# Kernel optimization log

Hardware: AMD Instinct MI355X
Metric: run time of the kernel (lower is better)

The kernel has to match this reference:

```python
import jax, jax.numpy as jnp
import numpy as np
from jax.scipy.linalg import cholesky, solve_triangular, cho_solve

N, M, D = 16384, 2048, 8
VAR, LS = 1.0, 0.5      # RBF kernel hyperparameters (same for kernel_f and kernel_g)
JITTER = 1e-6
BATCH_RATE = 1.0
HALF_LOG_2PI = 0.5 * float(np.log(2.0 * np.pi))


def rbf(x1, x2):
    # K[i,j] = VAR * exp(-||x1_i - x2_j||^2 / (2 LS^2))
    d2 = (jnp.sum(x1 * x1, 1)[:, None] + jnp.sum(x2 * x2, 1)[None, :]
          - 2.0 * (x1 @ x2.T))
    return VAR * jnp.exp(-0.5 * d2 / (LS * LS))


def setup_inputs() -> dict:
    key = jax.random.key(0)
    ks = jax.random.split(key, 7)
    x = jax.random.normal(ks[0], (N, D), dtype=jnp.float32)
    y = jax.random.normal(ks[1], (N, 1), dtype=jnp.float32)
    z = 2.0 * jax.random.uniform(ks[2], (M, D), dtype=jnp.float32) - 1.0  # inducing inputs in [-1,1]^D
    q_m_f = 0.5 * jax.random.normal(ks[3], (M, 1), dtype=jnp.float32)
    q_m_g = 0.5 * jax.random.normal(ks[4], (M, 1), dtype=jnp.float32)
    # Cholesky-like params: identity plus small strictly-lower noise -> PD covariance
    q_L_f = jnp.eye(M, dtype=jnp.float32) + 0.01 * jnp.tril(
        jax.random.normal(ks[5], (M, M), dtype=jnp.float32), -1)
    q_L_g = jnp.eye(M, dtype=jnp.float32) + 0.01 * jnp.tril(
        jax.random.normal(ks[6], (M, M), dtype=jnp.float32), -1)
    return {"x": x, "y": y, "z": z, "q_m_f": q_m_f, "q_L_f": q_L_f,
            "q_m_g": q_m_g, "q_L_g": q_L_g}


def _gp_marginals_and_kl(x, z, q_m, q_L_raw):
    """Marginal posterior mean/var at x and KL(q(u)||p(u)) for one sparse GP."""
    L_S = jnp.tril(q_L_raw)                     # [M,M]
    Kuu = rbf(z, z) + JITTER * jnp.eye(M, dtype=x.dtype)
    Lk = cholesky(Kuu, lower=True)
    Kfu = rbf(x, z)                             # [N,M]
    # A = Kfu @ Kuu^{-1}
    A = cho_solve((Lk, True), Kfu.T).T          # [N,M]
    m = (A @ q_m)[:, 0]                         # [N]
    # diag(Kff + A (S - Kuu) A^T) = diag(Kff) + diag(A S A^T) - diag(Kfu A^T)
    S = L_S @ L_S.T
    diag_Kff = jnp.full((x.shape[0],), VAR, dtype=x.dtype)
    v = diag_Kff + jnp.sum((A @ S) * A, axis=1) - jnp.sum(A * Kfu, axis=1)
    # KL(N(q_m, S) || N(0, Kuu))
    alpha = solve_triangular(Lk, q_m, lower=True)       # Kuu^{-1/2} m
    W = solve_triangular(Lk, L_S, lower=True)           # Kuu^{-1/2} L_S
    logdet_K = 2.0 * jnp.sum(jnp.log(jnp.diag(Lk)))
    logdet_S = 2.0 * jnp.sum(jnp.log(jnp.abs(jnp.diag(L_S))))
    kl = 0.5 * (jnp.sum(W * W) + jnp.sum(alpha * alpha)
                - jnp.asarray(M, x.dtype) + logdet_K - logdet_S)
    return m, v, kl


def reference(x, y, z, q_m_f, q_L_f, q_m_g, q_L_g):
    m_f, v_f, kl_f = _gp_marginals_and_kl(x, z, q_m_f, q_L_f)
    m_g, v_g, kl_g = _gp_marginals_and_kl(x, z, q_m_g, q_L_g)
    yv = y[:, 0]
    # HetGaussian variational expectation (Saul et al. 2016):
    # E_q[log N(y | f, exp(g))] per point
    expectation = (-HALF_LOG_2PI - 0.5 * m_g
                   - 0.5 * ((yv - m_f) ** 2 + v_f) * jnp.exp(-m_g + 0.5 * v_g))
    elbo = BATCH_RATE * jnp.sum(expectation) - (kl_f + kl_g)
    return -elbo
```

## Files before the change

### kernel.cpp

```cpp
#include <hip/hip_runtime.h>
#include <math.h>

#define NN 16384
#define MM 2048
#define DD 8
#define NB 32
#define GRIDN 256
#define SZB ((size_t)16777216)

constexpr float HLOG2PI = 0.91893853320467274178f;

using short8  = __attribute__((ext_vector_type(8))) short;
using float4v = __attribute__((ext_vector_type(4))) float;

__device__ __forceinline__ float4v f4zero(){ float4v v; v[0]=0.f; v[1]=0.f; v[2]=0.f; v[3]=0.f; return v; }

__device__ __forceinline__ void bfsplit(float v, short& h, short& lo){
  unsigned b = __float_as_uint(v);
  h = (short)(b >> 16);
  float hf = __uint_as_float(b & 0xFFFF0000u);
  lo = (short)(__float_as_uint(v - hf) >> 16);
}
__device__ __forceinline__ float bf2f(short s){
  return __uint_as_float(((unsigned)(unsigned short)s) << 16);
}
__device__ __forceinline__ float4v mfma3(short8 ah, short8 al, short8 bh, short8 bl, float4v c){
  c = __builtin_amdgcn_mfma_f32_16x16x32_bf16(ah, bh, c, 0, 0, 0);
  c = __builtin_amdgcn_mfma_f32_16x16x32_bf16(ah, bl, c, 0, 0, 0);
  c = __builtin_amdgcn_mfma_f32_16x16x32_bf16(al, bh, c, 0, 0, 0);
  return c;
}

__device__ __forceinline__ void gbar0(int* cnt, int* flag, int& gen){
  __syncthreads();
  if (threadIdx.x == 0){
    ++gen;
    __builtin_amdgcn_fence(__ATOMIC_RELEASE, "agent");
    int old = __hip_atomic_fetch_add(cnt, 1, __ATOMIC_RELAXED, __HIP_MEMORY_SCOPE_AGENT);
    if (old == gen*GRIDN - 1){
      __builtin_amdgcn_fence(__ATOMIC_ACQ_REL, "agent");
      __hip_atomic_store(flag, gen, __ATOMIC_RELAXED, __HIP_MEMORY_SCOPE_AGENT);
    } else {
      while (__hip_atomic_load(flag, __ATOMIC_RELAXED, __HIP_MEMORY_SCOPE_AGENT) < gen)
        __builtin_amdgcn_s_sleep(8);
    }
    __builtin_amdgcn_fence(__ATOMIC_ACQUIRE, "agent");
  }
  __syncthreads();
}

__device__ __forceinline__ void gbar_h(int* bar, int xcc, int myN, int nxcd, int& gen){
  __syncthreads();
  if (threadIdx.x == 0){
    ++gen;
    int* lcnt  = bar + xcc*32;
    int* lflag = bar + 512 + xcc*32;
    int* gcnt  = bar + 1024;
    int* gflag = bar + 1056;
    int old = __hip_atomic_fetch_add(lcnt, 1, __ATOMIC_RELAXED, __HIP_MEMORY_SCOPE_AGENT);
    if (old == gen*myN - 1){
      __builtin_amdgcn_fence(__ATOMIC_RELEASE, "agent");
      int g = __hip_atomic_fetch_add(gcnt, 1, __ATOMIC_RELAXED, __HIP_MEMORY_SCOPE_AGENT);
      if (g == gen*nxcd - 1){
        __hip_atomic_store(gflag, gen, __ATOMIC_RELAXED, __HIP_MEMORY_SCOPE_AGENT);
      } else {
        while (__hip_atomic_load(gflag, __ATOMIC_RELAXED, __HIP_MEMORY_SCOPE_AGENT) < gen)
          __builtin_amdgcn_s_sleep(8);
      }
      __builtin_amdgcn_fence(__ATOMIC_ACQUIRE, "agent");
      __hip_atomic_store(lflag, gen, __ATOMIC_RELAXED, __HIP_MEMORY_SCOPE_AGENT);
    } else {
      while (__hip_atomic_load(lflag, __ATOMIC_RELAXED, __HIP_MEMORY_SCOPE_AGENT) < gen)
        __builtin_amdgcn_s_sleep(8);
      __builtin_amdgcn_fence(__ATOMIC_ACQUIRE, "agent");
    }
  }
  __syncthreads();
}

__device__ __forceinline__ float block_reduce(float v, float* scratch){
  int lane = threadIdx.x & 63;
  int w    = threadIdx.x >> 6;
  #pragma unroll
  for (int off=32; off; off>>=1) v += __shfl_down(v, off, 64);
  __syncthreads();
  if (lane==0) scratch[w] = v;
  __syncthreads();
  float r = 0.f;
  if (threadIdx.x < 4) r = scratch[threadIdx.x];
  if (w==0){ r += __shfl_down(r, 2, 64); r += __shfl_down(r, 1, 64); }
  return r;
}

__device__ __forceinline__ void stage64(float (*S)[68], const float* __restrict__ g, int ld, int t){
  #pragma unroll
  for (int p=t; p<1024; p+=256)
    *(float4*)&S[p>>4][(p&15)*4] = *(const float4*)&g[(size_t)(p>>4)*ld + (p&15)*4];
}
__device__ __forceinline__ void tile_gemm_step(float acc[4][4], const float (*As)[68], const float (*Bs)[68], int tx, int ty){
  for (int k=0;k<64;++k){
    float ar[4], bc4[4];
    #pragma unroll
    for (int u=0;u<4;++u){ ar[u]=As[ty*4+u][k]; bc4[u]=Bs[k][tx*4+u]; }
    #pragma unroll
    for (int u=0;u<4;++u)
      #pragma unroll
      for (int v=0;v<4;++v) acc[u][v] += ar[u]*bc4[v];
  }
}
__device__ __forceinline__ void tile_syrk_step(float acc[4][4], const float (*P)[68], const float (*Q)[68], int tx, int ty){
  for (int k=0;k<64;++k){
    float pr[4], qc[4];
    #pragma unroll
    for (int u=0;u<4;++u){ pr[u]=P[ty*4+u][k]; qc[u]=Q[tx*4+u][k]; }
    #pragma unroll
    for (int u=0;u<4;++u)
      #pragma unroll
      for (int v=0;v<4;++v) acc[u][v] += pr[u]*qc[v];
  }
}

__device__ __forceinline__ void factor64_reg(const float (*S)[68],
    float* __restrict__ lkd, float* __restrict__ sdg_, int d, int t){
  if (t < 64){
    float xr[64];
    #pragma unroll
    for (int c4=0;c4<16;++c4) *(float4*)&xr[c4*4] = *(const float4*)&S[t][c4*4];
    float myrp = 1.f;
    #pragma unroll
    for (int j=0;j<64;++j){
      float ajj = __shfl(xr[j], j, 64);
      float piv = sqrtf(fmaxf(ajj, 1e-20f));
      float rp  = 1.f/piv;
      float val = xr[j]*rp;
      if (t==j){ xr[j] = piv; myrp = rp; }
      else if (t>j) xr[j] = val;
      else val = 0.f;
      #pragma unroll
      for (int c=j+1;c<64;++c){
        float vc = __shfl(val, c, 64);
        if (c<=t) xr[c] -= val*vc;
      }
    }
    #pragma unroll
    for (int c=0;c<64;++c) if (c>t) xr[c] = 0.f;
    #pragma unroll
    for (int c4=0;c4<16;++c4)
      *(float4*)&lkd[d*4096 + t*64 + c4*4] = *(float4*)&xr[c4*4];
    sdg_[d*64 + t] = myrp;
  }
}

__global__ __launch_bounds__(256) void factor_coop(
    const float* __restrict__ z,
    const float* __restrict__ qlf, const float* __restrict__ qlg,
    const float* __restrict__ qmf, const float* __restrict__ qmg,
    float* __restrict__ kuu, float* __restrict__ linv,
    float* __restrict__ wf, float* __restrict__ wg,
    float* __restrict__ af, float* __restrict__ ag,
    float* __restrict__ ptmp, float* __restrict__ lkdiag,
    float* __restrict__ sdg, float* __restrict__ ltri, int* __restrict__ bar)
{
  __shared__ float As[64][68];
  __shared__ float Bs[64][68];
  __shared__ float Cs[64][68];
  __shared__ float sd[64];
  __shared__ int binfo[2];
  const int bid = blockIdx.x, t = threadIdx.x;
  const int tx = t & 15, ty = t >> 4;

  int xcc_r;
  asm volatile("s_getreg_b32 %0, hwreg(HW_REG_XCC_ID)" : "=s"(xcc_r));
  const int xcc = xcc_r & 15;
  if (t == 0)
    __hip_atomic_fetch_add(bar + 1152 + xcc*32, 1, __ATOMIC_RELAXED, __HIP_MEMORY_SCOPE_AGENT);
  int gen0 = 0;
  gbar0(bar + 1088, bar + 1120, gen0);
  if (t == 0){
    int myN = __hip_atomic_load(bar + 1152 + xcc*32, __ATOMIC_RELAXED, __HIP_MEMORY_SCOPE_AGENT);
    int nx = 0;
    for (int i=0;i<16;++i)
      nx += (__hip_atomic_load(bar + 1152 + i*32, __ATOMIC_RELAXED, __HIP_MEMORY_SCOPE_AGENT) > 0);
    binfo[0] = myN; binfo[1] = nx;
  }
  __syncthreads();
  const int myN = binfo[0], nxcd = binfo[1];
  int gen = 0;

  if (bid == 0){
    for (int p=t; p<128; p+=256){ int i=p>>1, h=p&1;
      *(float4*)&As[i][h*4] = *(const float4*)&z[(size_t)i*DD + h*4]; }
    __syncthreads();
    float kv[4][4];
    #pragma unroll
    for (int u=0;u<4;++u)
      #pragma unroll
      for (int v=0;v<4;++v){
        float d2=0.f;
        #pragma unroll
        for (int d=0;d<8;++d){ float df=As[ty*4+u][d]-As[tx*4+v][d]; d2+=df*df; }
        kv[u][v] = __expf(-2.f*d2) + ((ty*4+u)==(tx*4+v) ? 1e-6f : 0.f);
      }
    __syncthreads();
    #pragma unroll
    for (int u=0;u<4;++u)
      #pragma unroll
      for (int v=0;v<4;++v) As[ty*4+u][tx*4+v] = kv[u][v];
    __syncthreads();
    factor64_reg(As, lkdiag, sdg, 0, t);
  } else {
    for (int idx=bid; idx<528; idx+=GRIDN-1){
      int r=0; while ((r+1)*(r+2)/2 <= idx) ++r;
      int c = idx - r*(r+1)/2;
      __syncthreads();
      for (int p=t; p<128; p+=256){ int i=p>>1, h=p&1;
        *(float4*)&As[i][h*4] = *(const float4*)&z[(size_t)(r*64+i)*DD + h*4];
        *(float4*)&Bs[i][h*4] = *(const float4*)&z[(size_t)(c*64+i)*DD + h*4]; }
      __syncthreads();
      #pragma unroll
      for (int u=0;u<4;++u){
        float4 o;
        float* ov = (float*)&o;
        #pragma unroll
        for (int v=0;v<4;++v){
          float d2=0.f;
          #pragma unroll
          for (int d=0;d<8;++d){ float df=As[ty*4+u][d]-Bs[tx*4+v][d]; d2+=df*df; }
          float val = __expf(-2.f*d2);
          if (r*64+ty*4+u == c*64+tx*4+v) val += 1e-6f;
          ov[v] = val;
        }
        *(float4*)&kuu[(size_t)(r*64+ty*4+u)*MM + c*64 + tx*4] = o;
      }
    }
  }
  gbar_h(bar, xcc, myN, nxcd, gen);

  for (int kb=0; kb<31; ++kb){
    int T = NB-1 - kb;
    int ntiles = T*(T+1)/2;
    if (bid < ntiles){
      stage64(Cs, lkdiag + kb*4096, 64, t);
      if (t < 64) sd[t] = sdg[kb*64 + t];
    }
    for (int idx=bid; idx<ntiles; idx+=GRIDN){
      int r=0; while ((r+1)*(r+2)/2 <= idx) ++r;
      int c = idx - r*(r+1)/2;
      int bi = kb+1+r, bc = kb+1+c;
      __syncthreads();
      stage64(As, kuu + (size_t)(bi*64)*MM + kb*64, MM, t);
      if (bc != bi) stage64(Bs, kuu + (size_t)(bc*64)*MM + kb*64, MM, t);
      __syncthreads();
      {
        int w = t>>6, l = t&63;
        if (w==0 || (w==1 && bc!=bi)){
          float (*S)[68] = (w==0)? As : Bs;
          float xr[64];
          #pragma unroll
          for (int c4=0;c4<16;++c4) *(float4*)&xr[c4*4] = *(const float4*)&S[l][c4*4];
          #pragma unroll
          for (int j=0;j<64;++j){
            float xj = xr[j]*sd[j];
            xr[j] = xj;
            #pragma unroll
            for (int cc=j+1;cc<64;++cc) xr[cc] -= xj*Cs[cc][j];
          }
          #pragma unroll
          for (int c4=0;c4<16;++c4) *(float4*)&S[l][c4*4] = *(float4*)&xr[c4*4];
        }
      }
      __syncthreads();
      if (bc == kb+1){
        for (int p=t;p<1024;p+=256)
          *(float4*)&ltri[(size_t)(bi*64+(p>>4))*MM + kb*64 + (p&15)*4] =
              *(float4*)&As[p>>4][(p&15)*4];
      }
      float acc[4][4] = {};
      tile_syrk_step(acc, As, (bc==bi)? As : Bs, tx, ty);
      if (bi==kb+1 && bc==kb+1){
        __syncthreads();
        #pragma unroll
        for (int u=0;u<4;++u)
          #pragma unroll
          for (int v=0;v<4;++v) Bs[ty*4+u][tx*4+v] = acc[u][v];
        __syncthreads();
        for (int p=t;p<1024;p+=256){
          int i=p>>4, c4=p&15;
          float4 kv = *(const float4*)&kuu[(size_t)(bi*64+i)*MM + bi*64 + c4*4];
          float4 bv = *(float4*)&Bs[i][c4*4];
          float4 o; o.x=kv.x-bv.x; o.y=kv.y-bv.y; o.z=kv.z-bv.z; o.w=kv.w-bv.w;
          *(float4*)&As[i][c4*4] = o;
        }
        __syncthreads();
        factor64_reg(As, lkdiag, sdg, kb+1, t);
      } else {
        #pragma unroll
        for (int u=0;u<4;++u){
          float4* dst = (float4*)&kuu[(size_t)(bi*64+ty*4+u)*MM + bc*64 + tx*4];
          float4 o = *dst;
          o.x-=acc[u][0]; o.y-=acc[u][1]; o.z-=acc[u][2]; o.w-=acc[u][3];
          *dst = o;
        }
      }
    }
    gbar_h(bar, xcc, myN, nxcd, gen);
  }

  if (bid < NB){
    stage64(As, lkdiag + bid*4096, 64, t);
    __syncthreads();
    if (t < 64){
      for (int j=0;j<64;++j){
        float s = (j==t)?1.f:0.f;
        for (int k=t;k<j;++k) s -= As[j][k]*Bs[k][t];
        Bs[j][t] = (j>=t)? s/As[j][j] : 0.f;
      }
    }
    __syncthreads();
    for (int p=t;p<1024;p+=256){ int i=p>>4, c4=p&15;
      *(float4*)&linv[(size_t)(bid*64+i)*MM + bid*64 + c4*4] = *(float4*)&Bs[i][c4*4]; }
  }
  gbar_h(bar, xcc, myN, nxcd, gen);

  for (int idx=bid; idx<16; idx+=GRIDN){
    int m = idx;
    __syncthreads();
    stage64(As, ltri + (size_t)((2*m+1)*64)*MM + (2*m)*64, MM, t);
    stage64(Bs, linv + (size_t)((2*m)*64)*MM   + (2*m)*64, MM, t);
    __syncthreads();
    float acc[4][4]={};
    tile_gemm_step(acc, As, Bs, tx, ty);
    __syncthreads();
    #pragma unroll
    for (int u=0;u<4;++u)
      #pragma unroll
      for (int v=0;v<4;++v) Bs[ty*4+u][tx*4+v] = acc[u][v];
    stage64(As, linv + (size_t)((2*m+1)*64)*MM + (2*m+1)*64, MM, t);
    __syncthreads();
    float o[4][4]={};
    tile_gemm_step(o, As, Bs, tx, ty);
    #pragma unroll
    for (int u=0;u<4;++u)
      *(float4*)&linv[(size_t)((2*m+1)*64+ty*4+u)*MM + (2*m)*64 + tx*4] =
          make_float4(-o[u][0],-o[u][1],-o[u][2],-o[u][3]);
  }
  gbar_h(bar, xcc, myN, nxcd, gen);

  for (int m=bid; m<8; m+=GRIDN){
    float* pm = ptmp + (size_t)m*128*128;
    for (int ti=0; ti<2; ++ti)
      for (int tj=0; tj<2; ++tj){
        int rb = m*4 + 2 + ti, cb0 = m*4;
        float acc[4][4]={};
        for (int k=tj; k<2; ++k){
          __syncthreads();
          stage64(As, ltri + (size_t)(rb*64)*MM + (cb0+k)*64, MM, t);
          stage64(Bs, linv + (size_t)((cb0+k)*64)*MM + (cb0+tj)*64, MM, t);
          __syncthreads();
          tile_gemm_step(acc, As, Bs, tx, ty);
        }
        #pragma unroll
        for (int u=0;u<4;++u)
          *(float4*)&pm[(size_t)(ti*64+ty*4+u)*128 + tj*64 + tx*4] =
              make_float4(acc[u][0],acc[u][1],acc[u][2],acc[u][3]);
      }
    for (int ti=0; ti<2; ++ti)
      for (int tj=0; tj<2; ++tj){
        int rb = m*4 + 2 + ti;
        float acc[4][4]={};
        for (int k=0; k<=ti; ++k){
          __syncthreads();
          stage64(As, linv + (size_t)(rb*64)*MM + (m*4+2+k)*64, MM, t);
          stage64(Bs, pm + (size_t)(k*64)*128 + tj*64, 128, t);
          __syncthreads();
          tile_gemm_step(acc, As, Bs, tx, ty);
        }
        #pragma unroll
        for (int u=0;u<4;++u)
          *(float4*)&linv[(size_t)(rb*64+ty*4+u)*MM + (m*4+tj)*64 + tx*4] =
              make_float4(-acc[u][0],-acc[u][1],-acc[u][2],-acc[u][3]);
      }
  }
  gbar_h(bar, xcc, myN, nxcd, gen);

  for (int s=2; s<5; ++s){
    int nb = 1<<s, mc = 16>>s, b = 64<<s;
    int tiles = mc*nb*nb;
    for (int idx=bid; idx<tiles; idx+=GRIDN){
      int m = idx/(nb*nb), r2 = idx%(nb*nb);
      int ti = r2/nb, tj = r2%nb;
      int rb = m*2*nb + nb + ti, cb0 = m*2*nb;
      float acc[4][4]={};
      for (int k=tj; k<nb; ++k){
        __syncthreads();
        stage64(As, ltri + (size_t)(rb*64)*MM + (cb0+k)*64, MM, t);
        stage64(Bs, linv + (size_t)((cb0+k)*64)*MM + (cb0+tj)*64, MM, t);
        __syncthreads();
        tile_gemm_step(acc, As, Bs, tx, ty);
      }
      float* pm = ptmp + (size_t)m*b*b;
      #pragma unroll
      for (int u=0;u<4;++u)
        *(float4*)&pm[(size_t)(ti*64+ty*4+u)*b + tj*64 + tx*4] =
            make_float4(acc[u][0],acc[u][1],acc[u][2],acc[u][3]);
    }
    gbar_h(bar, xcc, myN, nxcd, gen);
    for (int idx=bid; idx<tiles; idx+=GRIDN){
      int m = idx/(nb*nb), r2 = idx%(nb*nb);
      int ti = r2/nb, tj = r2%nb;
      int rb = m*2*nb + nb + ti;
      const float* pm = ptmp + (size_t)m*b*b;
      float acc[4][4]={};
      for (int k=0; k<=ti; ++k){
        __syncthreads();
        stage64(As, linv + (size_t)(rb*64)*MM + (m*2*nb+nb+k)*64, MM, t);
        stage64(Bs, pm + (size_t)(k*64)*b + tj*64, b, t);
        __syncthreads();
        tile_gemm_step(acc, As, Bs, tx, ty);
      }
      #pragma unroll
      for (int u=0;u<4;++u)
        *(float4*)&linv[(size_t)(rb*64+ty*4+u)*MM + (m*2*nb+tj)*64 + tx*4] =
            make_float4(-acc[u][0],-acc[u][1],-acc[u][2],-acc[u][3]);
    }
    gbar_h(bar, xcc, myN, nxcd, gen);
  }

  for (int idx=bid; idx<2*528; idx+=GRIDN){
    int gp = idx/528, rem = idx%528;
    int bi=0; while ((bi+1)*(bi+2)/2 <= rem) ++bi;
    int bj = rem - bi*(bi+1)/2;
    const float* ql = gp ? qlg : qlf;
    float* w        = gp ? wg  : wf;
    float acc[4][4]={};
    for (int bk=bj; bk<=bi; ++bk){
      __syncthreads();
      stage64(As, linv + (size_t)(bi*64)*MM + bk*64, MM, t);
      stage64(Bs, ql   + (size_t)(bk*64)*MM + bj*64, MM, t);
      __syncthreads();
      if (bk==bj){
        for (int p=t;p<4096;p+=256){ int i=p>>6, c=p&63; if (i<c) Bs[i][c]=0.f; }
        __syncthreads();
      }
      tile_gemm_step(acc, As, Bs, tx, ty);
    }
    #pragma unroll
    for (int u=0;u<4;++u)
      *(float4*)&w[(size_t)(bi*64+ty*4+u)*MM + bj*64 + tx*4] =
          make_float4(acc[u][0],acc[u][1],acc[u][2],acc[u][3]);
  }
  {
    int gw = bid*4 + (t>>6), l = t&63;
    for (int job=gw; job<4096; job+=GRIDN*4){
      int gp = job>>11, r = job&2047;
      const float* qm = gp ? qmg : qmf;
      float s=0.f;
      for (int c=l; c<=r; c+=64) s += linv[(size_t)r*MM+c]*qm[c];
      #pragma unroll
      for (int off=32; off; off>>=1) s += __shfl_down(s, off, 64);
      if (l==0) (gp ? ag : af)[r] = s;
    }
  }
}


__global__ __launch_bounds__(256) void zfrag_kernel(const float* __restrict__ z,
    short* __restrict__ zfh, short* __restrict__ zfl, float* __restrict__ zn2){
  int zr = blockIdx.x*256 + threadIdx.x;
  float v[DD]; float s = 0.f;
  #pragma unroll
  for (int d=0; d<DD; ++d){ v[d] = z[zr*DD + d]; s += v[d]*v[d]; }
  zn2[zr] = s;
  size_t base = (size_t)(zr >> 4)*512 + (zr & 15)*32;
  #pragma unroll
  for (int k=0; k<32; ++k){
    short h = 0, lo = 0;
    if (k < DD) bfsplit(v[k], h, lo);
    zfh[base + k] = h; zfl[base + k] = lo;
  }
}

__global__ __launch_bounds__(256) void red_small(const float* __restrict__ lkd,
    const float* __restrict__ qlf, const float* __restrict__ qlg,
    const float* __restrict__ af, const float* __restrict__ ag,
    float* __restrict__ scal){
  __shared__ float scratch[4];
  float ldk=0, ldf=0, ldg=0, a2f=0, a2g=0;
  for (int i=threadIdx.x;i<MM;i+=256){
    int kb = i>>6, r = i&63;
    ldk += __logf(lkd[kb*4096 + r*64 + r]);
    ldf += __logf(fabsf(qlf[(size_t)i*MM+i]));
    ldg += __logf(fabsf(qlg[(size_t)i*MM+i]));
    float v = af[i]; a2f += v*v;
    v = ag[i];       a2g += v*v;
  }
  float r;
  r = block_reduce(ldk, scratch); if (threadIdx.x==0) scal[0] = 2.f*r;
  r = block_reduce(ldf, scratch); if (threadIdx.x==0) scal[1] = 2.f*r;
  r = block_reduce(ldg, scratch); if (threadIdx.x==0) scal[2] = 2.f*r;
  r = block_reduce(a2f, scratch); if (threadIdx.x==0) scal[3] = r;
  r = block_reduce(a2g, scratch); if (threadIdx.x==0) scal[4] = r;
}

__global__ __launch_bounds__(256) void redw_kernel(const float* __restrict__ wf,
    const float* __restrict__ wg, float* __restrict__ scal){
  __shared__ float scratch[4];
  size_t start  = (size_t)blockIdx.x*256 + threadIdx.x;
  size_t stride = (size_t)gridDim.x*256;
  float sf=0, sg=0;
  for (size_t p=start;p<(size_t)MM*MM;p+=stride){
    float v=wf[p]; sf += v*v;
    v=wg[p];       sg += v*v;
  }
  float r = block_reduce(sf, scratch);
  if (threadIdx.x==0) atomicAdd(&scal[5], r);
  r = block_reduce(sg, scratch);
  if (threadIdx.x==0) atomicAdd(&scal[6], r);
}

__global__ void kl_kernel(const float* __restrict__ scal, float* __restrict__ out){
  float klf = 0.5f*(scal[5] + scal[3] - (float)MM + scal[0] - scal[1]);
  float klg = 0.5f*(scal[6] + scal[4] - (float)MM + scal[0] - scal[2]);
  out[0] += klf + klg;
}

__global__ __launch_bounds__(256) void split_rowmajor(const float* __restrict__ src,
    short* __restrict__ dh, short* __restrict__ dl){
  int p = blockIdx.x*256 + threadIdx.x;
  int chunk = p >> 9, wi = p & 511;
  int mo = chunk >> 6, ko = chunk & 63;
  int row = mo*16 + (wi >> 5), col = ko*32 + (wi & 31);
  float v = src[(size_t)row*MM + col];
  short h, lo; bfsplit(v, h, lo);
  dh[p] = h; dl[p] = lo;
}

__global__ __launch_bounds__(256) void split_transpose(const float* __restrict__ src,
    short* __restrict__ dh, short* __restrict__ dl){
  __shared__ float tile[32][33];
  int t = threadIdx.x;
  int mb = blockIdx.x, kb = blockIdx.y;
  #pragma unroll
  for (int k=0;k<4;++k){
    int idx = t + k*256;
    int lr = idx >> 5, lc = idx & 31;
    tile[lr][lc] = src[(size_t)(kb*32+lr)*MM + mb*32 + lc];
  }
  __syncthreads();
  #pragma unroll
  for (int e=0;e<4;++e){
    int p = t*4 + e;
    int c = p >> 9, wi = p & 511;
    int i = (wi >> 5) & 15, kk = wi & 31;
    float v = tile[kk][c*16 + i];
    short h, lo; bfsplit(v, h, lo);
    size_t gp = ((size_t)(mb*2 + c)*64 + kb)*512 + wi;
    dh[gp] = h; dl[gp] = lo;
  }
}

__global__ __launch_bounds__(256, 2) void tt_mfma(
    const float* __restrict__ x, const float* __restrict__ zn2,
    const short* __restrict__ zfh, const short* __restrict__ zfl,
    const short* __restrict__ lvh, const short* __restrict__ lvl,
    short* __restrict__ tth, short* __restrict__ ttl){
  __shared__ __align__(16) short lAh[8192], lAl[8192], lBh[8192], lBl[8192];
  int t = threadIdx.x;
  int l = t & 63, w = t >> 6;
  int istrip = blockIdx.x, bj2 = blockIdx.y;
  int li = l & 15, q = l >> 4;
  int lofs = li*32 + q*8;
  int wn4 = (w>>1)*4, wm4 = (w&1)*4;

  short8 xh[2], xl[2];
  float xn2v[8];
  {
    float xn2t[2];
    #pragma unroll
    for (int tn=0; tn<2; ++tn){
      int n = istrip*128 + w*32 + tn*16 + li;
      const float4* xp = (const float4*)(x + (size_t)n*DD);
      float4 p0 = xp[0], p1 = xp[1];
      float v[8] = {p0.x,p0.y,p0.z,p0.w,p1.x,p1.y,p1.z,p1.w};
      float s = 0.f;
      #pragma unroll
      for (int d=0; d<8; ++d) s += v[d]*v[d];
      xn2t[tn] = s;
      short8 hh, ll;
      #pragma unroll
      for (int j=0; j<8; ++j){
        short h=0, lo=0;
        if (q==0) bfsplit(v[j], h, lo);
        hh[j]=h; ll[j]=lo;
      }
      xh[tn]=hh; xl[tn]=ll;
    }
    #pragma unroll
    for (int tn=0; tn<2; ++tn)
      #pragma unroll
      for (int r=0; r<4; ++r)
        xn2v[tn*4+r] = __shfl(xn2t[tn], q*4 + r, 64);
  }

  float4v acc[4][4];
  #pragma unroll
  for (int i=0;i<4;++i)
    #pragma unroll
    for (int j=0;j<4;++j) acc[i][j] = f4zero();

  int nkt = 2*bj2 + 2;
  for (int bk=0; bk<nkt; ++bk){
    __syncthreads();
    {
      short8 zh[4], zl[4];
      float zt2[4];
      #pragma unroll
      for (int tz=0; tz<4; ++tz){
        size_t zo = (size_t)(bk*4 + tz)*512 + lofs;
        zh[tz] = *(const short8*)(zfh + zo);
        zl[tz] = *(const short8*)(zfl + zo);
        zt2[tz] = zn2[bk*64 + tz*16 + li];
      }
      #pragma unroll
      for (int tn=0; tn<2; ++tn){
        #pragma unroll
        for (int tz=0; tz<4; ++tz){
          float4v s4 = mfma3(xh[tn], xl[tn], zh[tz], zl[tz], f4zero());
          #pragma unroll
          for (int r=0; r<4; ++r){
            float e = __expf(4.f*s4[r] - 2.f*(xn2v[tn*4+r] + zt2[tz]));
            short h, lo; bfsplit(e, h, lo);
            int pos = ((w*2+tn)*2 + (tz>>1))*512 + (q*4+r)*32 + (tz&1)*16 + li;
            lAh[pos] = h; lAl[pos] = lo;
          }
        }
      }
    }
    #pragma unroll
    for (int c4 = t; c4 < 1024; c4 += 256){
      int ch = c4 >> 6, wdi = c4 & 63;
      size_t g = ((size_t)(bj2*8 + (ch>>1))*64 + (size_t)(bk*2 + (ch&1)))*64 + wdi;
      ((uint4*)lBh)[c4] = ((const uint4*)lvh)[g];
      ((uint4*)lBl)[c4] = ((const uint4*)lvl)[g];
    }
    __syncthreads();
    #pragma unroll
    for (int s=0; s<2; ++s){
      short8 ah[4], al[4], bh[4], bl[4];
      #pragma unroll
      for (int tn=0; tn<4; ++tn){
        int off = ((wn4+tn)*2 + s)*512 + lofs;
        ah[tn] = *(const short8*)&lAh[off];
        al[tn] = *(const short8*)&lAl[off];
      }
      #pragma unroll
      for (int tm=0; tm<4; ++tm){
        int off = ((wm4+tm)*2 + s)*512 + lofs;
        bh[tm] = *(const short8*)&lBh[off];
        bl[tm] = *(const short8*)&lBl[off];
      }
      #pragma unroll
      for (int tn=0; tn<4; ++tn)
        #pragma unroll
        for (int tm=0; tm<4; ++tm)
          acc[tn][tm] = mfma3(ah[tn], al[tn], bh[tm], bl[tm], acc[tn][tm]);
    }
  }
  #pragma unroll
  for (int tn=0; tn<4; ++tn){
    int no_g = istrip*8 + wn4 + tn;
    #pragma unroll
    for (int tm=0; tm<4; ++tm){
      int mo_g = bj2*4 + (w&1)*2 + (tm>>1);
      size_t cb = ((size_t)no_g*64 + mo_g)*512;
      #pragma unroll
      for (int r=0; r<4; ++r){
        short h, lo; bfsplit(acc[tn][tm][r], h, lo);
        size_t pos = cb + (q*4+r)*32 + (tm&1)*16 + li;
        tth[pos] = h; ttl[pos] = lo;
      }
    }
  }
}

__global__ __launch_bounds__(256) void lin_v2(const short* __restrict__ tth,
    const short* __restrict__ ttl, const float* __restrict__ af, const float* __restrict__ ag,
    float* __restrict__ t2, float* __restrict__ lf, float* __restrict__ lg){
  int t = threadIdx.x;
  int w = t >> 6, l = t & 63;
  int n = blockIdx.x*4 + w;
  int g = l >> 2, j = l & 3;
  float s2=0.f, sf=0.f, sg=0.f;
  #pragma unroll
  for (int it=0; it<4; ++it){
    int ck = g + it*16;
    size_t off = ((size_t)(n>>4)*64 + ck)*512 + (n&15)*32 + j*8;
    short8 h8 = *(const short8*)(tth + off);
    short8 l8 = *(const short8*)(ttl + off);
    int m0 = ck*32 + j*8;
    float4 a0 = *(const float4*)(af + m0), a1 = *(const float4*)(af + m0 + 4);
    float4 g0 = *(const float4*)(ag + m0), g1 = *(const float4*)(ag + m0 + 4);
    float av[8] = {a0.x,a0.y,a0.z,a0.w,a1.x,a1.y,a1.z,a1.w};
    float gv[8] = {g0.x,g0.y,g0.z,g0.w,g1.x,g1.y,g1.z,g1.w};
    #pragma unroll
    for (int e=0; e<8; ++e){
      float tv = bf2f(h8[e]) + bf2f(l8[e]);
      s2 += tv*tv; sf += tv*av[e]; sg += tv*gv[e];
    }
  }
  #pragma unroll
  for (int off=32; off; off>>=1){
    s2 += __shfl_down(s2, off, 64);
    sf += __shfl_down(sf, off, 64);
    sg += __shfl_down(sg, off, 64);
  }
  if (l==0){ t2[n] = s2; lf[n] = sf; lg[n] = sg; }
}

__global__ __launch_bounds__(256, 2) void quad_mfma(
    const short* __restrict__ tth, const short* __restrict__ ttl,
    const short* __restrict__ wfh, const short* __restrict__ wfl,
    const short* __restrict__ wgh, const short* __restrict__ wgl,
    float* __restrict__ vfq, float* __restrict__ vgq){
  __shared__ __align__(16) short lAh[8192], lAl[8192], lBh[8192], lBl[8192];
  int t = threadIdx.x, l = t & 63, w = t >> 6;
  int istrip = blockIdx.x, bj2 = blockIdx.y;
  const short* gbh = blockIdx.z ? wgh : wfh;
  const short* gbl = blockIdx.z ? wgl : wfl;
  float* vq = blockIdx.z ? vgq : vfq;
  int li = l & 15, q = l >> 4;
  int lofs = li*32 + q*8;
  int wn4 = (w>>1)*4, wm4 = (w&1)*4;

  float4v acc[4][4];
  #pragma unroll
  for (int i=0;i<4;++i)
    #pragma unroll
    for (int j=0;j<4;++j) acc[i][j] = f4zero();

  for (int bk=2*bj2; bk<32; ++bk){
    __syncthreads();
    #pragma unroll
    for (int c4 = t; c4 < 1024; c4 += 256){
      int ch = c4 >> 6, wdi = c4 & 63;
      size_t ga = ((size_t)(istrip*8 + (ch>>1))*64 + (size_t)(bk*2 + (ch&1)))*64 + wdi;
      ((uint4*)lAh)[c4] = ((const uint4*)tth)[ga];
      ((uint4*)lAl)[c4] = ((const uint4*)ttl)[ga];
      size_t gb = ((size_t)(bj2*8 + (ch>>1))*64 + (size_t)(bk*2 + (ch&1)))*64 + wdi;
      ((uint4*)lBh)[c4] = ((const uint4*)gbh)[gb];
      ((uint4*)lBl)[c4] = ((const uint4*)gbl)[gb];
    }
    __syncthreads();
    #pragma unroll
    for (int s=0; s<2; ++s){
      short8 ah[4], al[4], bh[4], bl[4];
      #pragma unroll
      for (int tn=0; tn<4; ++tn){
        int off = ((wn4+tn)*2 + s)*512 + lofs;
        ah[tn] = *(const short8*)&lAh[off];
        al[tn] = *(const short8*)&lAl[off];
      }
      #pragma unroll
      for (int tm=0; tm<4; ++tm){
        int off = ((wm4+tm)*2 + s)*512 + lofs;
        bh[tm] = *(const short8*)&lBh[off];
        bl[tm] = *(const short8*)&lBl[off];
      }
      #pragma unroll
      for (int tn=0; tn<4; ++tn)
        #pragma unroll
        for (int tm=0; tm<4; ++tm)
          acc[tn][tm] = mfma3(ah[tn], al[tn], bh[tm], bl[tm], acc[tn][tm]);
    }
  }
  float rs[16];
  #pragma unroll
  for (int tn=0; tn<4; ++tn)
    #pragma unroll
    for (int r=0; r<4; ++r){
      float s = 0.f;
      #pragma unroll
      for (int tm=0; tm<4; ++tm){ float v = acc[tn][tm][r]; s += v*v; }
      rs[tn*4+r] = s;
    }
  #pragma unroll
  for (int off=8; off; off>>=1)
    #pragma unroll
    for (int k=0; k<16; ++k) rs[k] += __shfl_down(rs[k], off, 16);
  if (li == 0){
    #pragma unroll
    for (int tn=0; tn<4; ++tn)
      #pragma unroll
      for (int r=0; r<4; ++r){
        int n = istrip*128 + (w>>1)*64 + tn*16 + q*4 + r;
        atomicAdd(&vq[n], rs[tn*4+r]);
      }
  }
}

__global__ __launch_bounds__(256) void final_kernel(const float* __restrict__ y,
    const float* __restrict__ t2, const float* __restrict__ lf, const float* __restrict__ lg,
    const float* __restrict__ vfq, const float* __restrict__ vgq, float* __restrict__ out){
  __shared__ float scratch[4];
  int i = blockIdx.x*256 + threadIdx.x;
  float mf = lf[i], mg = lg[i];
  float vf = 1.f + vfq[i] - t2[i];
  float vg = 1.f + vgq[i] - t2[i];
  float dy = y[i] - mf;
  float e = -HLOG2PI - 0.5f*mg - 0.5f*(dy*dy + vf)*__expf(-mg + 0.5f*vg);
  float r = block_reduce(e, scratch);
  if (threadIdx.x==0) atomicAdd(out, -r);
}

extern "C" void kernel_launch(void* const* d_in, const int* in_sizes, int n_in,
                              void* d_out, int out_size, void* d_ws, size_t ws_size,
                              hipStream_t stream){
  (void)in_sizes; (void)n_in; (void)out_size; (void)ws_size;
  const float* x   = (const float*)d_in[0];
  const float* y   = (const float*)d_in[1];
  const float* z   = (const float*)d_in[2];
  const float* qmf = (const float*)d_in[3];
  const float* qlf = (const float*)d_in[4];
  const float* qmg = (const float*)d_in[5];
  const float* qlg = (const float*)d_in[6];
  float* out = (float*)d_out;
  char* Bw = (char*)d_ws;

  float* kuu  = (float*)Bw;
  float* linv = (float*)(Bw + SZB);
  float* wf   = (float*)(Bw + 2*SZB);
  float* wg   = (float*)(Bw + 3*SZB);
  short* lvh  = (short*)Bw;
  short* lvl  = (short*)(Bw + SZB/2);
  short* wfh  = (short*)(Bw + SZB);
  short* wfl  = (short*)(Bw + SZB + SZB/2);
  short* wgh  = (short*)(Bw + 2*SZB);
  short* wgl  = (short*)(Bw + 2*SZB + SZB/2);
  short* tth  = (short*)(Bw + 3*SZB);
  short* ttl  = (short*)(Bw + 3*SZB + (size_t)NN*MM*2);
  float* ltri   = (float*)(Bw + 4*SZB);
  float* ptmp   = (float*)(Bw + 5*SZB);
  float* lkdiag = (float*)(Bw + 5*SZB + (size_t)4194304);
  float* sdg    = (float*)(Bw + 5*SZB + (size_t)4194304 + (size_t)524288);
  float* sm   = (float*)(Bw + 3*SZB + (size_t)NN*MM*4);
  float* af = sm;          float* ag = af + MM;
  float* t2 = ag + MM;     float* lf = t2 + NN;   float* lg = lf + NN;
  float* vfq = lg + NN;    float* vgq = vfq + NN; float* scal = vgq + NN;
  int*   bar = (int*)(scal + 64);
  float* zn2 = scal + 64 + 2048;
  short* zfh = (short*)(zn2 + MM);
  short* zfl = zfh + MM*32;

  hipMemsetAsync(out, 0, sizeof(float), stream);
  hipMemsetAsync(vfq, 0, (size_t)(2*NN + 64 + 2048)*sizeof(float), stream);
  hipMemsetAsync(wf,  0, 2*SZB, stream);
  hipMemsetAsync(linv,0, SZB,   stream);

  zfrag_kernel<<<MM/256, 256, 0, stream>>>(z, zfh, zfl, zn2);

  factor_coop<<<GRIDN, 256, 0, stream>>>(z, qlf, qlg, qmf, qmg,
                                         kuu, linv, wf, wg, af, ag,
                                         ptmp, lkdiag, sdg, ltri, bar);

  red_small<<<1, 256, 0, stream>>>(lkdiag, qlf, qlg, af, ag, scal);
  redw_kernel<<<512, 256, 0, stream>>>(wf, wg, scal);
  kl_kernel<<<1, 1, 0, stream>>>(scal, out);

  split_rowmajor<<<MM*MM/256, 256, 0, stream>>>(linv, lvh, lvl);
  split_transpose<<<dim3(MM/32, MM/32), 256, 0, stream>>>(wf, wfh, wfl);
  split_transpose<<<dim3(MM/32, MM/32), 256, 0, stream>>>(wg, wgh, wgl);

  tt_mfma<<<dim3(NN/128, MM/128), 256, 0, stream>>>(x, zn2, zfh, zfl, lvh, lvl, tth, ttl);
  lin_v2<<<NN/4, 256, 0, stream>>>(tth, ttl, af, ag, t2, lf, lg);
  quad_mfma<<<dim3(NN/128, MM/128, 2), 256, 0, stream>>>(tth, ttl, wfh, wfl, wgh, wgl, vfq, vgq);
  final_kernel<<<NN/256, 256, 0, stream>>>(y, t2, lf, lg, vfq, vgq, out);
}
```

Baseline: 4.267 ms.

## Replace fence-based grid barriers with agent-scope atomic loads and stores for shared data

Drops the agent-scope release/acquire fences from the cooperative grid barriers and instead routes cross-block data (Kuu tiles, diagonal factors, Linv, ltri, ptmp) through relaxed agent-scope 8-byte atomic loads and stores, with an explicit vmcnt wait before arriving at the barrier. The aim is to avoid the cache writeback/invalidate cost of the fences at each of the many barriers in the factorisation. The ptmp buffer is split into per-stage regions so one stage's scratch is never reused by the next, which moves lkdiag further out. The cost is that 16-byte vector accesses become pairs of 8-byte atomic accesses, and correctness now rests on the atomics bypassing non-coherent caches, which is subtle.

```diff
diff --git a/kernel.cpp b/kernel.cpp
--- a/kernel.cpp
+++ b/kernel.cpp
@@ -31,35 +31,48 @@
   return c;
 }
 
+union U8 { unsigned long long u; float f[2]; };
+
+__device__ __forceinline__ unsigned long long ald8(const float* p){
+  return __hip_atomic_load((const unsigned long long*)p, __ATOMIC_RELAXED, __HIP_MEMORY_SCOPE_AGENT);
+}
+__device__ __forceinline__ void ast8(float* p, unsigned long long v){
+  __hip_atomic_store((unsigned long long*)p, v, __ATOMIC_RELAXED, __HIP_MEMORY_SCOPE_AGENT);
+}
+__device__ __forceinline__ void ast8f(float* p, float a, float b){
+  U8 u; u.f[0]=a; u.f[1]=b;
+  __hip_atomic_store((unsigned long long*)p, u.u, __ATOMIC_RELAXED, __HIP_MEMORY_SCOPE_AGENT);
+}
+__device__ __forceinline__ void ast4(float* p, float v){
+  __hip_atomic_store(p, v, __ATOMIC_RELAXED, __HIP_MEMORY_SCOPE_AGENT);
+}
+
 __device__ __forceinline__ void gbar0(int* cnt, int* flag, int& gen){
   __syncthreads();
   if (threadIdx.x == 0){
     ++gen;
-    __builtin_amdgcn_fence(__ATOMIC_RELEASE, "agent");
     int old = __hip_atomic_fetch_add(cnt, 1, __ATOMIC_RELAXED, __HIP_MEMORY_SCOPE_AGENT);
     if (old == gen*GRIDN - 1){
-      __builtin_amdgcn_fence(__ATOMIC_ACQ_REL, "agent");
       __hip_atomic_store(flag, gen, __ATOMIC_RELAXED, __HIP_MEMORY_SCOPE_AGENT);
     } else {
       while (__hip_atomic_load(flag, __ATOMIC_RELAXED, __HIP_MEMORY_SCOPE_AGENT) < gen)
         __builtin_amdgcn_s_sleep(8);
     }
-    __builtin_amdgcn_fence(__ATOMIC_ACQUIRE, "agent");
   }
   __syncthreads();
 }
 
-__device__ __forceinline__ void gbar_h(int* bar, int xcc, int myN, int nxcd, int& gen){
+__device__ __forceinline__ void gbar_nf(int* bar, int xcc, int myN, int nxcd, int& gen){
   __syncthreads();
   if (threadIdx.x == 0){
     ++gen;
+    asm volatile("s_waitcnt vmcnt(0)" ::: "memory");
     int* lcnt  = bar + xcc*32;
     int* lflag = bar + 512 + xcc*32;
     int* gcnt  = bar + 1024;
     int* gflag = bar + 1056;
     int old = __hip_atomic_fetch_add(lcnt, 1, __ATOMIC_RELAXED, __HIP_MEMORY_SCOPE_AGENT);
     if (old == gen*myN - 1){
-      __builtin_amdgcn_fence(__ATOMIC_RELEASE, "agent");
       int g = __hip_atomic_fetch_add(gcnt, 1, __ATOMIC_RELAXED, __HIP_MEMORY_SCOPE_AGENT);
       if (g == gen*nxcd - 1){
         __hip_atomic_store(gflag, gen, __ATOMIC_RELAXED, __HIP_MEMORY_SCOPE_AGENT);
@@ -67,12 +80,10 @@
         while (__hip_atomic_load(gflag, __ATOMIC_RELAXED, __HIP_MEMORY_SCOPE_AGENT) < gen)
           __builtin_amdgcn_s_sleep(8);
       }
-      __builtin_amdgcn_fence(__ATOMIC_ACQUIRE, "agent");
       __hip_atomic_store(lflag, gen, __ATOMIC_RELAXED, __HIP_MEMORY_SCOPE_AGENT);
     } else {
       while (__hip_atomic_load(lflag, __ATOMIC_RELAXED, __HIP_MEMORY_SCOPE_AGENT) < gen)
         __builtin_amdgcn_s_sleep(8);
-      __builtin_amdgcn_fence(__ATOMIC_ACQUIRE, "agent");
     }
   }
   __syncthreads();
@@ -97,6 +108,16 @@
   for (int p=t; p<1024; p+=256)
     *(float4*)&S[p>>4][(p&15)*4] = *(const float4*)&g[(size_t)(p>>4)*ld + (p&15)*4];
 }
+__device__ __forceinline__ void stage64_a(float (*S)[68], const float* __restrict__ g, int ld, int t){
+  #pragma unroll
+  for (int p=t; p<1024; p+=256){
+    int r = p>>4, c0 = (p&15)*4;
+    const float* src = &g[(size_t)r*ld + c0];
+    unsigned long long v0 = ald8(src), v1 = ald8(src+2);
+    *(unsigned long long*)&S[r][c0]   = v0;
+    *(unsigned long long*)&S[r][c0+2] = v1;
+  }
+}
 __device__ __forceinline__ void tile_gemm_step(float acc[4][4], const float (*As)[68], const float (*Bs)[68], int tx, int ty){
   for (int k=0;k<64;++k){
     float ar[4], bc4[4];
@@ -145,9 +166,9 @@
     #pragma unroll
     for (int c=0;c<64;++c) if (c>t) xr[c] = 0.f;
     #pragma unroll
-    for (int c4=0;c4<16;++c4)
-      *(float4*)&lkd[d*4096 + t*64 + c4*4] = *(float4*)&xr[c4*4];
-    sdg_[d*64 + t] = myrp;
+    for (int c2=0;c2<32;++c2)
+      ast8f(&lkd[d*4096 + t*64 + c2*2], xr[c2*2], xr[c2*2+1]);
+    ast4(&sdg_[d*64 + t], myrp);
   }
 }
 
@@ -219,8 +240,7 @@
       __syncthreads();
       #pragma unroll
       for (int u=0;u<4;++u){
-        float4 o;
-        float* ov = (float*)&o;
+        float ov[4];
         #pragma unroll
         for (int v=0;v<4;++v){
           float d2=0.f;
@@ -230,11 +250,13 @@
           if (r*64+ty*4+u == c*64+tx*4+v) val += 1e-6f;
           ov[v] = val;
         }
-        *(float4*)&kuu[(size_t)(r*64+ty*4+u)*MM + c*64 + tx*4] = o;
-      }
-    }
-  }
-  gbar_h(bar, xcc, myN, nxcd, gen);
+        float* dst = &kuu[(size_t)(r*64+ty*4+u)*MM + c*64 + tx*4];
+        ast8f(dst,   ov[0], ov[1]);
+        ast8f(dst+2, ov[2], ov[3]);
+      }
+    }
+  }
+  gbar_nf(bar, xcc, myN, nxcd, gen);
 
   for (int kb=0; kb<31; ++kb){
     int T = NB-1 - kb;
@@ -248,8 +270,8 @@
       int c = idx - r*(r+1)/2;
       int bi = kb+1+r, bc = kb+1+c;
       __syncthreads();
-      stage64(As, kuu + (size_t)(bi*64)*MM + kb*64, MM, t);
-      if (bc != bi) stage64(Bs, kuu + (size_t)(bc*64)*MM + kb*64, MM, t);
+      stage64_a(As, kuu + (size_t)(bi*64)*MM + kb*64, MM, t);
+      if (bc != bi) stage64_a(Bs, kuu + (size_t)(bc*64)*MM + kb*64, MM, t);
       __syncthreads();
       {
         int w = t>>6, l = t&63;
@@ -271,9 +293,12 @@
       }
       __syncthreads();
       if (bc == kb+1){
-        for (int p=t;p<1024;p+=256)
-          *(float4*)&ltri[(size_t)(bi*64+(p>>4))*MM + kb*64 + (p&15)*4] =
-              *(float4*)&As[p>>4][(p&15)*4];
+        for (int p=t;p<1024;p+=256){
+          int rr=p>>4, c0=(p&15)*4;
+          float* dst = &ltri[(size_t)(bi*64+rr)*MM + kb*64 + c0];
+          ast8(dst,   *(const unsigned long long*)&As[rr][c0]);
+          ast8(dst+2, *(const unsigned long long*)&As[rr][c0+2]);
+        }
       }
       float acc[4][4] = {};
       tile_syrk_step(acc, As, (bc==bi)? As : Bs, tx, ty);
@@ -285,25 +310,27 @@
           for (int v=0;v<4;++v) Bs[ty*4+u][tx*4+v] = acc[u][v];
         __syncthreads();
         for (int p=t;p<1024;p+=256){
-          int i=p>>4, c4=p&15;
-          float4 kv = *(const float4*)&kuu[(size_t)(bi*64+i)*MM + bi*64 + c4*4];
-          float4 bv = *(float4*)&Bs[i][c4*4];
-          float4 o; o.x=kv.x-bv.x; o.y=kv.y-bv.y; o.z=kv.z-bv.z; o.w=kv.w-bv.w;
-          *(float4*)&As[i][c4*4] = o;
+          int i=p>>4, c0=(p&15)*4;
+          const float* kp = &kuu[(size_t)(bi*64+i)*MM + bi*64 + c0];
+          U8 k0,k1; k0.u=ald8(kp); k1.u=ald8(kp+2);
+          As[i][c0]   = k0.f[0]-Bs[i][c0];
+          As[i][c0+1] = k0.f[1]-Bs[i][c0+1];
+          As[i][c0+2] = k1.f[0]-Bs[i][c0+2];
+          As[i][c0+3] = k1.f[1]-Bs[i][c0+3];
         }
         __syncthreads();
         factor64_reg(As, lkdiag, sdg, kb+1, t);
       } else {
         #pragma unroll
         for (int u=0;u<4;++u){
-          float4* dst = (float4*)&kuu[(size_t)(bi*64+ty*4+u)*MM + bc*64 + tx*4];
-          float4 o = *dst;
-          o.x-=acc[u][0]; o.y-=acc[u][1]; o.z-=acc[u][2]; o.w-=acc[u][3];
-          *dst = o;
+          float* dst = &kuu[(size_t)(bi*64+ty*4+u)*MM + bc*64 + tx*4];
+          U8 p0,p1; p0.u=ald8(dst); p1.u=ald8(dst+2);
+          ast8f(dst,   p0.f[0]-acc[u][0], p0.f[1]-acc[u][1]);
+          ast8f(dst+2, p1.f[0]-acc[u][2], p1.f[1]-acc[u][3]);
         }
       }
     }
-    gbar_h(bar, xcc, myN, nxcd, gen);
+    gbar_nf(bar, xcc, myN, nxcd, gen);
   }
 
   if (bid < NB){
@@ -317,10 +344,12 @@
       }
     }
     __syncthreads();
-    for (int p=t;p<1024;p+=256){ int i=p>>4, c4=p&15;
-      *(float4*)&linv[(size_t)(bid*64+i)*MM + bid*64 + c4*4] = *(float4*)&Bs[i][c4*4]; }
-  }
-  gbar_h(bar, xcc, myN, nxcd, gen);
+    for (int p=t;p<1024;p+=256){ int i=p>>4, c0=(p&15)*4;
+      float* dst = &linv[(size_t)(bid*64+i)*MM + bid*64 + c0];
+      ast8(dst,   *(const unsigned long long*)&Bs[i][c0]);
+      ast8(dst+2, *(const unsigned long long*)&Bs[i][c0+2]); }
+  }
+  gbar_nf(bar, xcc, myN, nxcd, gen);
 
   for (int idx=bid; idx<16; idx+=GRIDN){
     int m = idx;
@@ -340,11 +369,13 @@
     float o[4][4]={};
     tile_gemm_step(o, As, Bs, tx, ty);
     #pragma unroll
-    for (int u=0;u<4;++u)
-      *(float4*)&linv[(size_t)((2*m+1)*64+ty*4+u)*MM + (2*m)*64 + tx*4] =
-          make_float4(-o[u][0],-o[u][1],-o[u][2],-o[u][3]);
-  }
-  gbar_h(bar, xcc, myN, nxcd, gen);
+    for (int u=0;u<4;++u){
+      float* dst = &linv[(size_t)((2*m+1)*64+ty*4+u)*MM + (2*m)*64 + tx*4];
+      ast8f(dst,   -o[u][0], -o[u][1]);
+      ast8f(dst+2, -o[u][2], -o[u][3]);
+    }
+  }
+  gbar_nf(bar, xcc, myN, nxcd, gen);
 
   for (int m=bid; m<8; m+=GRIDN){
     float* pm = ptmp + (size_t)m*128*128;
@@ -376,15 +407,18 @@
           tile_gemm_step(acc, As, Bs, tx, ty);
         }
         #pragma unroll
-        for (int u=0;u<4;++u)
-          *(float4*)&linv[(size_t)(rb*64+ty*4+u)*MM + (m*4+tj)*64 + tx*4] =
-              make_float4(-acc[u][0],-acc[u][1],-acc[u][2],-acc[u][3]);
-      }
-  }
-  gbar_h(bar, xcc, myN, nxcd, gen);
+        for (int u=0;u<4;++u){
+          float* dst = &linv[(size_t)(rb*64+ty*4+u)*MM + (m*4+tj)*64 + tx*4];
+          ast8f(dst,   -acc[u][0], -acc[u][1]);
+          ast8f(dst+2, -acc[u][2], -acc[u][3]);
+        }
+      }
+  }
+  gbar_nf(bar, xcc, myN, nxcd, gen);
 
   for (int s=2; s<5; ++s){
     int nb = 1<<s, mc = 16>>s, b = 64<<s;
+    float* pmb = ptmp + (s==2 ? 131072 : (s==3 ? 393216 : 917504));
     int tiles = mc*nb*nb;
     for (int idx=bid; idx<tiles; idx+=GRIDN){
       int m = idx/(nb*nb), r2 = idx%(nb*nb);
@@ -398,18 +432,20 @@
         __syncthreads();
         tile_gemm_step(acc, As, Bs, tx, ty);
       }
-      float* pm = ptmp + (size_t)m*b*b;
-      #pragma unroll
-      for (int u=0;u<4;++u)
-        *(float4*)&pm[(size_t)(ti*64+ty*4+u)*b + tj*64 + tx*4] =
-            make_float4(acc[u][0],acc[u][1],acc[u][2],acc[u][3]);
-    }
-    gbar_h(bar, xcc, myN, nxcd, gen);
+      float* pm = pmb + (size_t)m*b*b;
+      #pragma unroll
+      for (int u=0;u<4;++u){
+        float* dst = &pm[(size_t)(ti*64+ty*4+u)*b + tj*64 + tx*4];
+        ast8f(dst,   acc[u][0], acc[u][1]);
+        ast8f(dst+2, acc[u][2], acc[u][3]);
+      }
+    }
+    gbar_nf(bar, xcc, myN, nxcd, gen);
     for (int idx=bid; idx<tiles; idx+=GRIDN){
       int m = idx/(nb*nb), r2 = idx%(nb*nb);
       int ti = r2/nb, tj = r2%nb;
       int rb = m*2*nb + nb + ti;
-      const float* pm = ptmp + (size_t)m*b*b;
+      const float* pm = pmb + (size_t)m*b*b;
       float acc[4][4]={};
       for (int k=0; k<=ti; ++k){
         __syncthreads();
@@ -419,11 +455,13 @@
         tile_gemm_step(acc, As, Bs, tx, ty);
       }
       #pragma unroll
-      for (int u=0;u<4;++u)
-        *(float4*)&linv[(size_t)(rb*64+ty*4+u)*MM + (m*2*nb+tj)*64 + tx*4] =
-            make_float4(-acc[u][0],-acc[u][1],-acc[u][2],-acc[u][3]);
-    }
-    gbar_h(bar, xcc, myN, nxcd, gen);
+      for (int u=0;u<4;++u){
+        float* dst = &linv[(size_t)(rb*64+ty*4+u)*MM + (m*2*nb+tj)*64 + tx*4];
+        ast8f(dst,   -acc[u][0], -acc[u][1]);
+        ast8f(dst+2, -acc[u][2], -acc[u][3]);
+      }
+    }
+    gbar_nf(bar, xcc, myN, nxcd, gen);
   }
 
   for (int idx=bid; idx<2*528; idx+=GRIDN){
@@ -840,8 +878,8 @@
   short* ttl  = (short*)(Bw + 3*SZB + (size_t)NN*MM*2);
   float* ltri   = (float*)(Bw + 4*SZB);
   float* ptmp   = (float*)(Bw + 5*SZB);
-  float* lkdiag = (float*)(Bw + 5*SZB + (size_t)4194304);
-  float* sdg    = (float*)(Bw + 5*SZB + (size_t)4194304 + (size_t)524288);
+  float* lkdiag = (float*)(Bw + 5*SZB + (size_t)8388608);
+  float* sdg    = (float*)(Bw + 5*SZB + (size_t)8388608 + (size_t)524288);
   float* sm   = (float*)(Bw + 3*SZB + (size_t)NN*MM*4);
   float* af = sm;          float* ag = af + MM;
   float* t2 = ag + MM;     float* lf = t2 + NN;   float* lg = lf + NN;
```

New measurement: 4.496 ms. +5.4%, slower.

## Vectorize LDS tile GEMM/SYRK, block the triangular solve, rebalance Cholesky tile scheduling

Applied to the files above, without the earlier changes.

The inner GEMM and SYRK tile loops now read float4 vectors from shared memory four k-steps at a time, replacing scalar LDS reads. The per-row triangular solve in the panel update is blocked by four columns, using float4 reads of the diagonal block. In the blocked Cholesky loop, block 0 now handles only its first tile (the diagonal factorization) and the remaining tiles are spread over the other blocks. Each recursion level of the inverse also gets its own ptmp region, with lkdiag moved further out to make room, likely so stages do not overwrite each other's temporaries. The changes aim to cut LDS instruction count and the critical-path load on block 0, at the cost of a different summation order and more workspace.

```diff
diff --git a/kernel.cpp b/kernel.cpp
--- a/kernel.cpp
+++ b/kernel.cpp
@@ -98,25 +98,35 @@
     *(float4*)&S[p>>4][(p&15)*4] = *(const float4*)&g[(size_t)(p>>4)*ld + (p&15)*4];
 }
 __device__ __forceinline__ void tile_gemm_step(float acc[4][4], const float (*As)[68], const float (*Bs)[68], int tx, int ty){
-  for (int k=0;k<64;++k){
-    float ar[4], bc4[4];
-    #pragma unroll
-    for (int u=0;u<4;++u){ ar[u]=As[ty*4+u][k]; bc4[u]=Bs[k][tx*4+u]; }
-    #pragma unroll
-    for (int u=0;u<4;++u)
-      #pragma unroll
-      for (int v=0;v<4;++v) acc[u][v] += ar[u]*bc4[v];
+  for (int k=0;k<64;k+=4){
+    float4 b0 = *(const float4*)&Bs[k  ][tx*4];
+    float4 b1 = *(const float4*)&Bs[k+1][tx*4];
+    float4 b2 = *(const float4*)&Bs[k+2][tx*4];
+    float4 b3 = *(const float4*)&Bs[k+3][tx*4];
+    #pragma unroll
+    for (int u=0;u<4;++u){
+      float4 a = *(const float4*)&As[ty*4+u][k];
+      acc[u][0] += a.x*b0.x + a.y*b1.x + a.z*b2.x + a.w*b3.x;
+      acc[u][1] += a.x*b0.y + a.y*b1.y + a.z*b2.y + a.w*b3.y;
+      acc[u][2] += a.x*b0.z + a.y*b1.z + a.z*b2.z + a.w*b3.z;
+      acc[u][3] += a.x*b0.w + a.y*b1.w + a.z*b2.w + a.w*b3.w;
+    }
   }
 }
 __device__ __forceinline__ void tile_syrk_step(float acc[4][4], const float (*P)[68], const float (*Q)[68], int tx, int ty){
-  for (int k=0;k<64;++k){
-    float pr[4], qc[4];
-    #pragma unroll
-    for (int u=0;u<4;++u){ pr[u]=P[ty*4+u][k]; qc[u]=Q[tx*4+u][k]; }
-    #pragma unroll
-    for (int u=0;u<4;++u)
-      #pragma unroll
-      for (int v=0;v<4;++v) acc[u][v] += pr[u]*qc[v];
+  for (int k=0;k<64;k+=4){
+    float4 q0 = *(const float4*)&Q[tx*4  ][k];
+    float4 q1 = *(const float4*)&Q[tx*4+1][k];
+    float4 q2 = *(const float4*)&Q[tx*4+2][k];
+    float4 q3 = *(const float4*)&Q[tx*4+3][k];
+    #pragma unroll
+    for (int u=0;u<4;++u){
+      float4 p = *(const float4*)&P[ty*4+u][k];
+      acc[u][0] += p.x*q0.x + p.y*q0.y + p.z*q0.z + p.w*q0.w;
+      acc[u][1] += p.x*q1.x + p.y*q1.y + p.z*q1.z + p.w*q1.w;
+      acc[u][2] += p.x*q2.x + p.y*q2.y + p.z*q2.z + p.w*q2.w;
+      acc[u][3] += p.x*q3.x + p.y*q3.y + p.z*q3.z + p.w*q3.w;
+    }
   }
 }
 
@@ -243,7 +253,8 @@
       stage64(Cs, lkdiag + kb*4096, 64, t);
       if (t < 64) sd[t] = sdg[kb*64 + t];
     }
-    for (int idx=bid; idx<ntiles; idx+=GRIDN){
+    int idx = bid;
+    while (idx < ntiles){
       int r=0; while ((r+1)*(r+2)/2 <= idx) ++r;
       int c = idx - r*(r+1)/2;
       int bi = kb+1+r, bc = kb+1+c;
@@ -259,11 +270,17 @@
           #pragma unroll
           for (int c4=0;c4<16;++c4) *(float4*)&xr[c4*4] = *(const float4*)&S[l][c4*4];
           #pragma unroll
-          for (int j=0;j<64;++j){
-            float xj = xr[j]*sd[j];
-            xr[j] = xj;
+          for (int j=0;j<64;j+=4){
+            float x0 =  xr[j  ]*sd[j];
+            float x1 = (xr[j+1] - x0*Cs[j+1][j])*sd[j+1];
+            float x2 = (xr[j+2] - x0*Cs[j+2][j] - x1*Cs[j+2][j+1])*sd[j+2];
+            float x3 = (xr[j+3] - x0*Cs[j+3][j] - x1*Cs[j+3][j+1] - x2*Cs[j+3][j+2])*sd[j+3];
+            xr[j]=x0; xr[j+1]=x1; xr[j+2]=x2; xr[j+3]=x3;
             #pragma unroll
-            for (int cc=j+1;cc<64;++cc) xr[cc] -= xj*Cs[cc][j];
+            for (int cc=j+4; cc<64; ++cc){
+              float4 c4v = *(const float4*)&Cs[cc][j];
+              xr[cc] -= x0*c4v.x + x1*c4v.y + x2*c4v.z + x3*c4v.w;
+            }
           }
           #pragma unroll
           for (int c4=0;c4<16;++c4) *(float4*)&S[l][c4*4] = *(float4*)&xr[c4*4];
@@ -302,6 +319,8 @@
           *dst = o;
         }
       }
+      if (bid == 0) break;
+      idx = (idx < GRIDN) ? (GRIDN - 1 + bid) : (idx + GRIDN - 1);
     }
     gbar_h(bar, xcc, myN, nxcd, gen);
   }
@@ -385,6 +404,7 @@
 
   for (int s=2; s<5; ++s){
     int nb = 1<<s, mc = 16>>s, b = 64<<s;
+    float* pmb = ptmp + (s==2 ? 131072 : (s==3 ? 393216 : 917504));
     int tiles = mc*nb*nb;
     for (int idx=bid; idx<tiles; idx+=GRIDN){
       int m = idx/(nb*nb), r2 = idx%(nb*nb);
@@ -398,7 +418,7 @@
         __syncthreads();
         tile_gemm_step(acc, As, Bs, tx, ty);
       }
-      float* pm = ptmp + (size_t)m*b*b;
+      float* pm = pmb + (size_t)m*b*b;
       #pragma unroll
       for (int u=0;u<4;++u)
         *(float4*)&pm[(size_t)(ti*64+ty*4+u)*b + tj*64 + tx*4] =
@@ -409,7 +429,7 @@
       int m = idx/(nb*nb), r2 = idx%(nb*nb);
       int ti = r2/nb, tj = r2%nb;
       int rb = m*2*nb + nb + ti;
-      const float* pm = ptmp + (size_t)m*b*b;
+      const float* pm = pmb + (size_t)m*b*b;
       float acc[4][4]={};
       for (int k=0; k<=ti; ++k){
         __syncthreads();
@@ -840,8 +860,8 @@
   short* ttl  = (short*)(Bw + 3*SZB + (size_t)NN*MM*2);
   float* ltri   = (float*)(Bw + 4*SZB);
   float* ptmp   = (float*)(Bw + 5*SZB);
-  float* lkdiag = (float*)(Bw + 5*SZB + (size_t)4194304);
-  float* sdg    = (float*)(Bw + 5*SZB + (size_t)4194304 + (size_t)524288);
+  float* lkdiag = (float*)(Bw + 5*SZB + (size_t)8388608);
+  float* sdg    = (float*)(Bw + 5*SZB + (size_t)8388608 + (size_t)524288);
   float* sm   = (float*)(Bw + 3*SZB + (size_t)NN*MM*4);
   float* af = sm;          float* ag = af + MM;
   float* t2 = ag + MM;     float* lf = t2 + NN;   float* lg = lf + NN;
```

Result: slower. 5.017 ms (+17.6%).
